# Performance work log

Measured on AMD Instinct MI355X. Metric: run time of the kernel, lower is better.

## Reference

```python
import jax, jax.numpy as jnp
import numpy as np

K_NEIGHBORS = 32  # nsample

def setup_inputs() -> dict:
    key = jax.random.key(0)
    ks = jax.random.split(key, 16)
    B, C, N = 4, 3, 4096
    def w(k, shape):
        return jax.random.normal(k, shape, dtype=jnp.float32) * 0.05
    inp = {"x": jax.random.normal(ks[0], (B, C, N), dtype=jnp.float32)}
    # three scale MLPs share shapes -> stack along leading scale axis (s=3)
    inp["sW0"] = w(ks[1], (3, 64, 3));    inp["sb0"] = w(ks[2], (3, 64))
    inp["sW1"] = w(ks[3], (3, 64, 64));   inp["sb1"] = w(ks[4], (3, 64))
    inp["sW2"] = w(ks[5], (3, 128, 64));  inp["sb2"] = w(ks[6], (3, 128))
    inp["gW0"] = w(ks[7], (256, 384));    inp["gb0"] = w(ks[8], (256,))
    inp["gW1"] = w(ks[9], (1024, 256));   inp["gb1"] = w(ks[10], (1024,))
    inp["mW0"] = w(ks[11], (256, 1024));  inp["mb0"] = w(ks[12], (256,))
    inp["mW1"] = w(ks[13], (128, 256));   inp["mb1"] = w(ks[14], (128,))
    return inp

def _knn_idx(x, k):
    # x: [B, 3, N] channels-first points; k nearest neighbors excluding self
    pts = jnp.swapaxes(x, 1, 2)                       # [B, N, 3]
    sq = jnp.sum(pts * pts, axis=-1)                  # [B, N]
    d = sq[:, :, None] + sq[:, None, :] - 2.0 * jnp.einsum('bnc,bmc->bnm', pts, pts)
    _, idx = jax.lax.top_k(-d, k + 1)                 # nearest first (self at 0)
    return idx[:, :, 1:]                              # [B, N, k]

def reference(x, sW0, sb0, sW1, sb1, sW2, sb2, gW0, gb0, gW1, gb1, mW0, mb0, mW1, mb1):
    B, C, N = x.shape
    # radius is unused by sample_and_group_knn -> all three scales share knn idx
    idx = _knn_idx(x, K_NEIGHBORS)                    # [B, N, K]
    # gather: per-batch x[:, idx[b]] -> [B, C, N, K]
    g = jax.vmap(lambda xf, i: xf[:, i])(x, idx)
    # three shared-weight 1x1-conv MLPs, batched over scale axis s
    h = jax.nn.relu(jnp.einsum('bcnk,soc->sbonk', g, sW0) + sb0[:, None, :, None, None])
    h = jax.nn.relu(jnp.einsum('sbcnk,soc->sbonk', h, sW1) + sb1[:, None, :, None, None])
    h = jax.nn.relu(jnp.einsum('sbcnk,soc->sbonk', h, sW2) + sb2[:, None, :, None, None])
    p = jnp.max(h, axis=-1)                           # [3, B, 128, N] max over neighbors
    point = jnp.moveaxis(p, 0, 1).reshape(B, 3 * p.shape[2], N)  # concat scales -> [B, 384, N]
    gf = jax.nn.relu(jnp.einsum('bcn,oc->bon', point, gW0) + gb0[None, :, None])
    gf = jax.nn.relu(jnp.einsum('bcn,oc->bon', gf, gW1) + gb1[None, :, None])     # [B,1024,N]
    msf = jax.nn.relu(jnp.einsum('bcn,oc->bon', gf, mW0) + mb0[None, :, None])
    msf = jax.nn.relu(jnp.einsum('bcn,oc->bon', msf, mW1) + mb1[None, :, None])   # [B,128,N]
    global_feature = jnp.max(gf, axis=-1)             # [B, 1024]
    return (global_feature, msf)
```

## Files before the change

### kernel.cpp

```cpp
#include <hip/hip_runtime.h>
#include <hip/hip_bf16.h>

#define NPTS 4096
#define KNN  32

typedef __attribute__((ext_vector_type(8))) short short8;
typedef __attribute__((ext_vector_type(4))) float floatx4;
typedef unsigned short u16x2 __attribute__((ext_vector_type(2)));

__device__ __forceinline__ unsigned short f2bf(float f) {
    unsigned u = __float_as_uint(f);
    u = (u + 0x7FFFu + ((u >> 16) & 1u)) >> 16;
    return (unsigned short)u;
}

__global__ __launch_bounds__(256) void prep_all(
    const float* __restrict__ x, float4* __restrict__ pts4,
    const float* __restrict__ gW0, const float* __restrict__ gW1,
    const float* __restrict__ mW0, const float* __restrict__ mW1,
    unsigned short* __restrict__ Wb0, unsigned short* __restrict__ Wb1,
    unsigned short* __restrict__ Wb2, unsigned short* __restrict__ Wb3)
{
    const int blk = blockIdx.x, t = threadIdx.x;
    if (blk < 64) {
        const int i = blk * 256 + t;
        const int b = i >> 12, n = i & (NPTS - 1);
        const float* xb = x + (size_t)b * 3 * NPTS;
        const float qx = xb[n], qy = xb[NPTS + n], qz = xb[2 * NPTS + n];
        pts4[i] = make_float4(qx, qy, qz, qx * qx + qy * qy + qz * qz);
    } else {
        const int wi = (blk - 64) * 256 + t;
        float v; unsigned short* dst;
        if (wi < 98304)       { v = gW0[wi];          dst = Wb0 + wi; }
        else if (wi < 360448) { v = gW1[wi - 98304];  dst = Wb1 + (wi - 98304); }
        else if (wi < 622592) { v = mW0[wi - 360448]; dst = Wb2 + (wi - 360448); }
        else                  { v = mW1[wi - 622592]; dst = Wb3 + (wi - 622592); }
        *dst = f2bf(v);
    }
}

__global__ __launch_bounds__(256) void knn_kernel12(const float4* __restrict__ pts4,
                                                    int* __restrict__ knn_out)
{
    __shared__ unsigned sred[2][4];
    __shared__ unsigned long long C[256];
    __shared__ unsigned ccnt;

    const int t = threadIdx.x, wid = t >> 6, lane = t & 63;
    const int q = blockIdx.x, b = q >> 12, n = q & (NPTS - 1);
    const float4* P = pts4 + ((size_t)b << 12);
    const float4 s = P[n];
    const float px = s.x, py = s.y, pz = s.z, sqn = s.w;

    if (t == 0) ccnt = 0u;

    unsigned key[16];
    #pragma unroll
    for (int g = 0; g < 4; ++g) {
        float4 c0 = P[((g * 4 + 0) << 8) + t];
        float4 c1 = P[((g * 4 + 1) << 8) + t];
        float4 c2 = P[((g * 4 + 2) << 8) + t];
        float4 c3 = P[((g * 4 + 3) << 8) + t];
        float d0 = (sqn + c0.w) - 2.0f * (px * c0.x + py * c0.y + pz * c0.z);
        float d1 = (sqn + c1.w) - 2.0f * (px * c1.x + py * c1.y + pz * c1.z);
        float d2 = (sqn + c2.w) - 2.0f * (px * c2.x + py * c2.y + pz * c2.z);
        float d3 = (sqn + c3.w) - 2.0f * (px * c3.x + py * c3.y + pz * c3.z);
        unsigned u0 = __float_as_uint(d0), u1 = __float_as_uint(d1);
        unsigned u2 = __float_as_uint(d2), u3 = __float_as_uint(d3);
        key[g * 4 + 0] = (u0 & 0x80000000u) ? ~u0 : (u0 | 0x80000000u);
        key[g * 4 + 1] = (u1 & 0x80000000u) ? ~u1 : (u1 | 0x80000000u);
        key[g * 4 + 2] = (u2 & 0x80000000u) ? ~u2 : (u2 | 0x80000000u);
        key[g * 4 + 3] = (u3 & 0x80000000u) ? ~u3 : (u3 | 0x80000000u);
    }

    int pp = 0;
    auto countLE = [&](unsigned thr) -> unsigned {
        unsigned c = 0;
        #pragma unroll
        for (int r = 0; r < 16; ++r)
            c += (unsigned)__popcll(__ballot(key[r] <= thr));
        if (lane == 0) sred[pp & 1][wid] = c;
        __syncthreads();
        const unsigned g = sred[pp & 1][0] + sred[pp & 1][1] +
                           sred[pp & 1][2] + sred[pp & 1][3];
        ++pp;
        return g;
    };

    unsigned lo = 0x100u, hi = 0x1FEu;
    for (int it = 0; it < 8; ++it) {
        const unsigned mid = (lo + hi) >> 1;
        const unsigned g = countLE((mid << 23) | 0x7FFFFFu);
        if (g >= 33u) hi = mid; else lo = mid + 1u;
    }
    unsigned loK = lo << 23;
    unsigned hiK = (lo << 23) | 0x7FFFFFu;
    unsigned cntF = countLE(hiK);
    while (cntF > 256u && loK < hiK) {
        const unsigned midK = loK + ((hiK - loK) >> 1);
        const unsigned c = countLE(midK);
        if (c >= 33u) { hiK = midK; cntF = c; } else loK = midK + 1u;
    }
    const unsigned thrF = hiK;

    #pragma unroll
    for (int r = 0; r < 16; ++r) {
        if (key[r] <= thrF) {
            unsigned p = atomicAdd(&ccnt, 1u);
            if (p < 256u)
                C[p] = ((unsigned long long)key[r] << 32) |
                       (unsigned)((r << 8) + t);
        }
    }
    __syncthreads();

    int nc = (int)ccnt; if (nc > 256) nc = 256;
    if (t < nc) {
        const unsigned long long me = C[t];
        int rank = 0;
        for (int j = 0; j < nc; ++j) rank += (C[j] < me) ? 1 : 0;
        if (rank >= 1 && rank <= KNN)
            knn_out[(size_t)q * KNN + (rank - 1)] = (int)(me & 0xFFFFFFFFu);
    }
}

__global__ __launch_bounds__(256) void pointmlp_kernel(
    const float* __restrict__ x,
    const float* __restrict__ sW0, const float* __restrict__ sb0,
    const float* __restrict__ sW1, const float* __restrict__ sb1,
    const float* __restrict__ sW2, const float* __restrict__ sb2,
    unsigned short* __restrict__ F)
{
    __shared__ __align__(16) float BUF[8192];
    __shared__ __align__(16) float h1s[64 * 36];
    __shared__ float b1s[64];
    __shared__ float b2s[128];
    __shared__ float pts[3 * 33];

    const int t = threadIdx.x;
    const int s = blockIdx.y;
    const int tile = blockIdx.x;
    const int b = tile >> 7;
    const int j0 = (tile & 127) << 5;
    const float* xb = x + (size_t)b * 3 * NPTS;

    if (t < 192) BUF[t] = sW0[s * 192 + t];
    else if (t < 256) BUF[t] = sb0[s * 64 + (t - 192)];
    if (t < 64) b1s[t] = sb1[s * 64 + t];
    if (t < 128) b2s[t] = sb2[s * 128 + t];
    if (t < 96) { int c = t >> 5, p = t & 31; pts[c * 33 + p] = xb[c * NPTS + j0 + p]; }
    {
        const float* W1 = sW1 + (size_t)s * 4096;
        int o = t & 63, q = t >> 6;
        #pragma unroll
        for (int r = 0; r < 4; ++r) {
            float4 w = *(const float4*)(W1 + o * 64 + q * 16 + r * 4);
            int i = q * 16 + r * 4;
            BUF[256 + (i + 0) * 64 + o] = w.x;
            BUF[256 + (i + 1) * 64 + o] = w.y;
            BUF[256 + (i + 2) * 64 + o] = w.z;
            BUF[256 + (i + 3) * 64 + o] = w.w;
        }
    }
    __syncthreads();
    const int o = t & 63, pg = t >> 6;
    float* h0 = BUF + 4352;
    {
        float w0 = BUF[o * 3], w1 = BUF[o * 3 + 1], w2 = BUF[o * 3 + 2], bb = BUF[192 + o];
        #pragma unroll
        for (int p = 0; p < 8; ++p) {
            int pp = pg * 8 + p;
            float a = bb + w0 * pts[pp] + w1 * pts[33 + pp] + w2 * pts[66 + pp];
            h0[o * 36 + pp] = fmaxf(a, 0.0f);
        }
    }
    __syncthreads();
    {
        float acc[8];
        #pragma unroll
        for (int p = 0; p < 8; ++p) acc[p] = b1s[o];
        for (int i = 0; i < 64; ++i) {
            float w = BUF[256 + i * 64 + o];
            float4 ha = *(const float4*)&h0[i * 36 + pg * 8];
            float4 hb = *(const float4*)&h0[i * 36 + pg * 8 + 4];
            acc[0] += w * ha.x; acc[1] += w * ha.y; acc[2] += w * ha.z; acc[3] += w * ha.w;
            acc[4] += w * hb.x; acc[5] += w * hb.y; acc[6] += w * hb.z; acc[7] += w * hb.w;
        }
        #pragma unroll
        for (int p = 0; p < 8; ++p) h1s[o * 36 + pg * 8 + p] = fmaxf(acc[p], 0.0f);
    }
    __syncthreads();
    {
        const float* W2 = sW2 + (size_t)s * 8192;
        int o2 = t & 127, q = t >> 7;
        #pragma unroll
        for (int r = 0; r < 8; ++r) {
            float4 w = *(const float4*)(W2 + o2 * 64 + q * 32 + r * 4);
            int i = q * 32 + r * 4;
            BUF[(i + 0) * 128 + o2] = w.x;
            BUF[(i + 1) * 128 + o2] = w.y;
            BUF[(i + 2) * 128 + o2] = w.z;
            BUF[(i + 3) * 128 + o2] = w.w;
        }
    }
    __syncthreads();
    {
        int o2 = t & 127, ph = t >> 7;
        float acc[16];
        #pragma unroll
        for (int p = 0; p < 16; ++p) acc[p] = b2s[o2];
        for (int i = 0; i < 64; ++i) {
            float w = BUF[i * 128 + o2];
            float4 ha = *(const float4*)&h1s[i * 36 + ph * 16];
            float4 hb = *(const float4*)&h1s[i * 36 + ph * 16 + 4];
            float4 hc = *(const float4*)&h1s[i * 36 + ph * 16 + 8];
            float4 hd = *(const float4*)&h1s[i * 36 + ph * 16 + 12];
            acc[0]  += w * ha.x; acc[1]  += w * ha.y; acc[2]  += w * ha.z; acc[3]  += w * ha.w;
            acc[4]  += w * hb.x; acc[5]  += w * hb.y; acc[6]  += w * hb.z; acc[7]  += w * hb.w;
            acc[8]  += w * hc.x; acc[9]  += w * hc.y; acc[10] += w * hc.z; acc[11] += w * hc.w;
            acc[12] += w * hd.x; acc[13] += w * hd.y; acc[14] += w * hd.z; acc[15] += w * hd.w;
        }
        #pragma unroll
        for (int p = 0; p < 16; ++p) {
            int j = j0 + ph * 16 + p;
            F[((size_t)b * NPTS + j) * 384 + s * 128 + o2] = f2bf(fmaxf(acc[p], 0.0f));
        }
    }
}

__global__ __launch_bounds__(192) void maxgather_bf16(
    const unsigned short* __restrict__ F, const int* __restrict__ knn,
    unsigned short* __restrict__ pt)
{
    __shared__ int idxS[KNN];
    const int q = blockIdx.x;
    const int b = q >> 12;
    const int t = threadIdx.x;
    if (t < KNN) idxS[t] = knn[(size_t)q * KNN + t];
    __syncthreads();
    const unsigned short* Fb = F + (size_t)b * NPTS * 384 + t * 2;
    u16x2 m = (u16x2)0;
    #pragma unroll 8
    for (int k = 0; k < KNN; ++k) {
        u16x2 v = *(const u16x2*)(Fb + (size_t)idxS[k] * 384);
        m = __builtin_elementwise_max(m, v);
    }
    *(u16x2*)(pt + (size_t)q * 384 + t * 2) = m;
}

template<int DO_ROWMAX>
__global__ __launch_bounds__(256) void gemm_bf16(
    const unsigned short* __restrict__ Wb, const unsigned short* __restrict__ Bt,
    const float* __restrict__ bias, void* __restrict__ outp,
    float* __restrict__ gfeat, int M, int K)
{
    __shared__ __align__(16) unsigned short As[128 * 40];
    __shared__ __align__(16) unsigned short Bs[128 * 40];
    __shared__ float biasS[128];
    __shared__ int redI[128];

    const int t = threadIdx.x;
    const int b = blockIdx.z;
    const int m0 = blockIdx.x * 128;
    const int n0 = blockIdx.y * 128;
    if (t < 128) biasS[t] = bias[m0 + t];
    if (DO_ROWMAX && t < 128) redI[t] = 0;

    const int wave = t >> 6, lane = t & 63, quad = lane >> 4, l15 = lane & 15;
    const int wr = wave >> 1, wc = wave & 1;

    const int am = t & 127, akh = t >> 7;
    const unsigned short* Wp = Wb + (size_t)(m0 + am) * K + akh * 16;
    const int bn = t >> 2, bq = t & 3;
    const unsigned short* Bp = Bt + ((size_t)b * NPTS + n0) * K;

    floatx4 acc[16];
    #pragma unroll
    for (int i = 0; i < 16; ++i) acc[i] = (floatx4){0.f, 0.f, 0.f, 0.f};

    const int nk = K >> 5;
    for (int kt = 0; kt < nk; ++kt) {
        const int k0 = kt << 5;
        uint4 av0 = *(const uint4*)(Wp + k0);
        uint4 av1 = *(const uint4*)(Wp + k0 + 8);
        uint4 bv0 = *(const uint4*)(Bp + (size_t)bn * K + k0 + bq * 8);
        uint4 bv1 = *(const uint4*)(Bp + (size_t)(bn + 64) * K + k0 + bq * 8);
        __syncthreads();
        {
            uint4* dst = (uint4*)&As[am * 40 + akh * 16];
            dst[0] = av0;
            dst[1] = av1;
            *(uint4*)&Bs[bn * 40 + bq * 8] = bv0;
            *(uint4*)&Bs[(bn + 64) * 40 + bq * 8] = bv1;
        }
        __syncthreads();
        short8 af[4], bfv[4];
        #pragma unroll
        for (int i = 0; i < 4; ++i)
            af[i] = *(const short8*)&As[(wr * 64 + i * 16 + l15) * 40 + quad * 8];
        #pragma unroll
        for (int j = 0; j < 4; ++j)
            bfv[j] = *(const short8*)&Bs[(wc * 64 + j * 16 + l15) * 40 + quad * 8];
        #pragma unroll
        for (int i = 0; i < 4; ++i)
            #pragma unroll
            for (int j = 0; j < 4; ++j)
                acc[i * 4 + j] = __builtin_amdgcn_mfma_f32_16x16x32_bf16(
                    af[i], bfv[j], acc[i * 4 + j], 0, 0, 0);
    }

    #pragma unroll
    for (int i = 0; i < 4; ++i) {
        const int mbase = wr * 64 + i * 16 + quad * 4;
        float rm0 = 0.f, rm1 = 0.f, rm2 = 0.f, rm3 = 0.f;
        #pragma unroll
        for (int j = 0; j < 4; ++j) {
            const int n = n0 + wc * 64 + j * 16 + l15;
            float v0 = fmaxf(acc[i * 4 + j][0] + biasS[mbase + 0], 0.f);
            float v1 = fmaxf(acc[i * 4 + j][1] + biasS[mbase + 1], 0.f);
            float v2 = fmaxf(acc[i * 4 + j][2] + biasS[mbase + 2], 0.f);
            float v3 = fmaxf(acc[i * 4 + j][3] + biasS[mbase + 3], 0.f);
            if (DO_ROWMAX) {
                rm0 = fmaxf(rm0, v0); rm1 = fmaxf(rm1, v1);
                rm2 = fmaxf(rm2, v2); rm3 = fmaxf(rm3, v3);
            }
            ushort4 pk;
            pk.x = f2bf(v0); pk.y = f2bf(v1); pk.z = f2bf(v2); pk.w = f2bf(v3);
            *(ushort4*)((unsigned short*)outp +
                        ((size_t)b * NPTS + n) * M + m0 + mbase) = pk;
        }
        if (DO_ROWMAX) {
            atomicMax(&redI[mbase + 0], __float_as_int(rm0));
            atomicMax(&redI[mbase + 1], __float_as_int(rm1));
            atomicMax(&redI[mbase + 2], __float_as_int(rm2));
            atomicMax(&redI[mbase + 3], __float_as_int(rm3));
        }
    }
    if (DO_ROWMAX) {
        __syncthreads();
        if (t < 128)
            atomicMax((int*)&gfeat[(size_t)b * 1024 + m0 + t], redI[t]);
    }
}

__global__ __launch_bounds__(256) void fused_head(
    const unsigned short* __restrict__ Wb2, const unsigned short* __restrict__ Wb3,
    const float* __restrict__ mb0, const float* __restrict__ mb1,
    const unsigned short* __restrict__ gft, float* __restrict__ outp)
{
    __shared__ __align__(16) unsigned short As[256 * 40];
    __shared__ __align__(16) unsigned short Bs[64 * 40];
    __shared__ __align__(16) unsigned short H[64 * 264];
    __shared__ float b0s[256];
    __shared__ float b1s[128];

    const int t = threadIdx.x;
    const int n0 = blockIdx.x * 64;
    const int b = blockIdx.y;
    b0s[t] = mb0[t];
    if (t < 128) b1s[t] = mb1[t];

    const int wave = t >> 6, lane = t & 63, quad = lane >> 4, l15 = lane & 15;

    const unsigned short* Ap = Wb2 + (size_t)t * 1024;
    const int bn = t >> 2, bq = t & 3;
    const unsigned short* Bp = gft + ((size_t)b * NPTS + n0) * 1024;

    floatx4 acc[16];
    #pragma unroll
    for (int i = 0; i < 16; ++i) acc[i] = (floatx4){0.f, 0.f, 0.f, 0.f};

    for (int kt = 0; kt < 32; ++kt) {
        const int k0 = kt << 5;
        uint4 a0 = *(const uint4*)(Ap + k0);
        uint4 a1 = *(const uint4*)(Ap + k0 + 8);
        uint4 a2 = *(const uint4*)(Ap + k0 + 16);
        uint4 a3 = *(const uint4*)(Ap + k0 + 24);
        uint4 bv = *(const uint4*)(Bp + (size_t)bn * 1024 + k0 + bq * 8);
        __syncthreads();
        *(uint4*)&As[t * 40 + 0]  = a0;
        *(uint4*)&As[t * 40 + 8]  = a1;
        *(uint4*)&As[t * 40 + 16] = a2;
        *(uint4*)&As[t * 40 + 24] = a3;
        *(uint4*)&Bs[bn * 40 + bq * 8] = bv;
        __syncthreads();
        short8 af[4], bfv[4];
        #pragma unroll
        for (int i = 0; i < 4; ++i)
            af[i] = *(const short8*)&As[(wave * 64 + i * 16 + l15) * 40 + quad * 8];
        #pragma unroll
        for (int j = 0; j < 4; ++j)
            bfv[j] = *(const short8*)&Bs[(j * 16 + l15) * 40 + quad * 8];
        #pragma unroll
        for (int i = 0; i < 4; ++i)
            #pragma unroll
            for (int j = 0; j < 4; ++j)
                acc[i * 4 + j] = __builtin_amdgcn_mfma_f32_16x16x32_bf16(
                    af[i], bfv[j], acc[i * 4 + j], 0, 0, 0);
    }
    #pragma unroll
    for (int i = 0; i < 4; ++i) {
        const int mbase = wave * 64 + i * 16 + quad * 4;
        #pragma unroll
        for (int j = 0; j < 4; ++j) {
            const int nl = j * 16 + l15;
            ushort4 pk;
            pk.x = f2bf(fmaxf(acc[i * 4 + j][0] + b0s[mbase + 0], 0.f));
            pk.y = f2bf(fmaxf(acc[i * 4 + j][1] + b0s[mbase + 1], 0.f));
            pk.z = f2bf(fmaxf(acc[i * 4 + j][2] + b0s[mbase + 2], 0.f));
            pk.w = f2bf(fmaxf(acc[i * 4 + j][3] + b0s[mbase + 3], 0.f));
            *(ushort4*)&H[nl * 264 + mbase] = pk;
        }
    }

    floatx4 acc2[8];
    #pragma unroll
    for (int i = 0; i < 8; ++i) acc2[i] = (floatx4){0.f, 0.f, 0.f, 0.f};
    const int am2 = t & 127, ah = t >> 7;

    for (int kt = 0; kt < 8; ++kt) {
        const int k0 = kt << 5;
        uint4 a0 = *(const uint4*)(Wb3 + (size_t)am2 * 256 + k0 + ah * 16);
        uint4 a1 = *(const uint4*)(Wb3 + (size_t)am2 * 256 + k0 + ah * 16 + 8);
        __syncthreads();
        *(uint4*)&As[am2 * 40 + ah * 16]     = a0;
        *(uint4*)&As[am2 * 40 + ah * 16 + 8] = a1;
        __syncthreads();
        short8 af2[2], bf2[4];
        #pragma unroll
        for (int i = 0; i < 2; ++i)
            af2[i] = *(const short8*)&As[(wave * 32 + i * 16 + l15) * 40 + quad * 8];
        #pragma unroll
        for (int j = 0; j < 4; ++j)
            bf2[j] = *(const short8*)&H[(j * 16 + l15) * 264 + k0 + quad * 8];
        #pragma unroll
        for (int i = 0; i < 2; ++i)
            #pragma unroll
            for (int j = 0; j < 4; ++j)
                acc2[i * 4 + j] = __builtin_amdgcn_mfma_f32_16x16x32_bf16(
                    af2[i], bf2[j], acc2[i * 4 + j], 0, 0, 0);
    }
    #pragma unroll
    for (int i = 0; i < 2; ++i) {
        const int m2 = wave * 32 + i * 16 + quad * 4;
        #pragma unroll
        for (int j = 0; j < 4; ++j) {
            const int n = n0 + j * 16 + l15;
            float* o = outp + ((size_t)b * 128 + m2) * NPTS + n;
            o[0 * NPTS] = fmaxf(acc2[i * 4 + j][0] + b1s[m2 + 0], 0.f);
            o[1 * NPTS] = fmaxf(acc2[i * 4 + j][1] + b1s[m2 + 1], 0.f);
            o[2 * NPTS] = fmaxf(acc2[i * 4 + j][2] + b1s[m2 + 2], 0.f);
            o[3 * NPTS] = fmaxf(acc2[i * 4 + j][3] + b1s[m2 + 3], 0.f);
        }
    }
}

extern "C" void kernel_launch(void* const* d_in, const int* in_sizes, int n_in,
                              void* d_out, int out_size, void* d_ws, size_t ws_size,
                              hipStream_t stream)
{
    const float* x   = (const float*)d_in[0];
    const float* sW0 = (const float*)d_in[1];
    const float* sb0 = (const float*)d_in[2];
    const float* sW1 = (const float*)d_in[3];
    const float* sb1 = (const float*)d_in[4];
    const float* sW2 = (const float*)d_in[5];
    const float* sb2 = (const float*)d_in[6];
    const float* gW0 = (const float*)d_in[7];
    const float* gb0 = (const float*)d_in[8];
    const float* gW1 = (const float*)d_in[9];
    const float* gb1 = (const float*)d_in[10];
    const float* mW0 = (const float*)d_in[11];
    const float* mb0 = (const float*)d_in[12];
    const float* mW1 = (const float*)d_in[13];
    const float* mb1 = (const float*)d_in[14];
    float* outp = (float*)d_out;

    char* ws = (char*)d_ws;
    int*            idx     = (int*)(ws);
    float4*         pts4    = (float4*)(ws + 2097152u);
    unsigned short* Wb0     = (unsigned short*)(ws + 2359296u);
    unsigned short* Wb1     = (unsigned short*)(ws + 2555904u);
    unsigned short* Wb2     = (unsigned short*)(ws + 3080192u);
    unsigned short* Wb3     = (unsigned short*)(ws + 3604480u);
    unsigned short* F       = (unsigned short*)(ws + 4194304u);
    unsigned short* point_t = (unsigned short*)(ws + 18874368u);
    unsigned short* gf0t    = (unsigned short*)(ws + 33554432u);
    unsigned short* gft     = (unsigned short*)(ws + 50331648u);

    prep_all<<<dim3(2624), dim3(256), 0, stream>>>(
        x, pts4, gW0, gW1, mW0, mW1, Wb0, Wb1, Wb2, Wb3);
    knn_kernel12<<<dim3(16384), dim3(256), 0, stream>>>(pts4, idx);
    pointmlp_kernel<<<dim3(512, 3), dim3(256), 0, stream>>>(
        x, sW0, sb0, sW1, sb1, sW2, sb2, F);
    maxgather_bf16<<<dim3(16384), dim3(192), 0, stream>>>(F, idx, point_t);
    gemm_bf16<0><<<dim3(2, 32, 4), dim3(256), 0, stream>>>(
        Wb0, point_t, gb0, gf0t, nullptr, 256, 384);
    gemm_bf16<1><<<dim3(8, 32, 4), dim3(256), 0, stream>>>(
        Wb1, gf0t, gb1, gft, outp, 1024, 256);
    fused_head<<<dim3(64, 4), dim3(256), 0, stream>>>(
        Wb2, Wb3, mb0, mb1, gft, outp + 4096);
}
```

Before: 286.8 us.

## Port per-point MLP to bf16 MFMA and reuse KNN bisection count

The per-point scale MLP layers 1 and 2 now run on bf16 MFMA 16x16x32 instructions. The weights are converted to bf16 once in the prep kernel and staged in padded LDS tiles, replacing the scalar fp32 FMA loops. Separately, the KNN radix bisection reuses the count it recorded at the upper bound instead of issuing one more counting pass. The MLP change cuts compute and LDS traffic, at the cost of bf16 rounding of intermediate activations.

```diff
diff --git a/kernel.cpp b/kernel.cpp
--- a/kernel.cpp
+++ b/kernel.cpp
@@ -18,8 +18,10 @@
     const float* __restrict__ x, float4* __restrict__ pts4,
     const float* __restrict__ gW0, const float* __restrict__ gW1,
     const float* __restrict__ mW0, const float* __restrict__ mW1,
+    const float* __restrict__ sW1, const float* __restrict__ sW2,
     unsigned short* __restrict__ Wb0, unsigned short* __restrict__ Wb1,
-    unsigned short* __restrict__ Wb2, unsigned short* __restrict__ Wb3)
+    unsigned short* __restrict__ Wb2, unsigned short* __restrict__ Wb3,
+    unsigned short* __restrict__ Wb4, unsigned short* __restrict__ Wb5)
 {
     const int blk = blockIdx.x, t = threadIdx.x;
     if (blk < 64) {
@@ -34,12 +36,14 @@
         if (wi < 98304)       { v = gW0[wi];          dst = Wb0 + wi; }
         else if (wi < 360448) { v = gW1[wi - 98304];  dst = Wb1 + (wi - 98304); }
         else if (wi < 622592) { v = mW0[wi - 360448]; dst = Wb2 + (wi - 360448); }
-        else                  { v = mW1[wi - 622592]; dst = Wb3 + (wi - 622592); }
+        else if (wi < 655360) { v = mW1[wi - 622592]; dst = Wb3 + (wi - 622592); }
+        else if (wi < 667648) { v = sW1[wi - 655360]; dst = Wb4 + (wi - 655360); }
+        else                  { v = sW2[wi - 667648]; dst = Wb5 + (wi - 667648); }
         *dst = f2bf(v);
     }
 }
 
-__global__ __launch_bounds__(256) void knn_kernel12(const float4* __restrict__ pts4,
+__global__ __launch_bounds__(256) void knn_kernel13(const float4* __restrict__ pts4,
                                                     int* __restrict__ knn_out)
 {
     __shared__ unsigned sred[2][4];
@@ -87,15 +91,15 @@
         return g;
     };
 
-    unsigned lo = 0x100u, hi = 0x1FEu;
+    unsigned lo = 0x100u, hi = 0x1FEu, cntHi = 4096u;
     for (int it = 0; it < 8; ++it) {
         const unsigned mid = (lo + hi) >> 1;
         const unsigned g = countLE((mid << 23) | 0x7FFFFFu);
-        if (g >= 33u) hi = mid; else lo = mid + 1u;
+        if (g >= 33u) { hi = mid; cntHi = g; } else lo = mid + 1u;
     }
     unsigned loK = lo << 23;
     unsigned hiK = (lo << 23) | 0x7FFFFFu;
-    unsigned cntF = countLE(hiK);
+    unsigned cntF = cntHi;
     while (cntF > 256u && loK < hiK) {
         const unsigned midK = loK + ((hiK - loK) >> 1);
         const unsigned c = countLE(midK);
@@ -124,17 +128,19 @@
     }
 }
 
-__global__ __launch_bounds__(256) void pointmlp_kernel(
+__global__ __launch_bounds__(256) void pointmlp_mfma(
     const float* __restrict__ x,
     const float* __restrict__ sW0, const float* __restrict__ sb0,
-    const float* __restrict__ sW1, const float* __restrict__ sb1,
-    const float* __restrict__ sW2, const float* __restrict__ sb2,
+    const unsigned short* __restrict__ W1b, const float* __restrict__ sb1,
+    const unsigned short* __restrict__ W2b, const float* __restrict__ sb2,
     unsigned short* __restrict__ F)
 {
-    __shared__ __align__(16) float BUF[8192];
-    __shared__ __align__(16) float h1s[64 * 36];
-    __shared__ float b1s[64];
-    __shared__ float b2s[128];
+    __shared__ __align__(16) unsigned short W1s[64 * 72];
+    __shared__ __align__(16) unsigned short W2s[128 * 72];
+    __shared__ __align__(16) unsigned short h0T[32 * 72];
+    __shared__ __align__(16) unsigned short h1T[32 * 72];
+    __shared__ float W0s[192];
+    __shared__ float b0s[64], b1s[64], b2s[128];
     __shared__ float pts[3 * 33];
 
     const int t = threadIdx.x;
@@ -144,86 +150,88 @@
     const int j0 = (tile & 127) << 5;
     const float* xb = x + (size_t)b * 3 * NPTS;
 
-    if (t < 192) BUF[t] = sW0[s * 192 + t];
-    else if (t < 256) BUF[t] = sb0[s * 64 + (t - 192)];
-    if (t < 64) b1s[t] = sb1[s * 64 + t];
+    if (t < 192) W0s[t] = sW0[s * 192 + t];
+    if (t < 64) b0s[t] = sb0[s * 64 + t];
+    if (t >= 64 && t < 128) b1s[t - 64] = sb1[s * 64 + (t - 64)];
     if (t < 128) b2s[t] = sb2[s * 128 + t];
     if (t < 96) { int c = t >> 5, p = t & 31; pts[c * 33 + p] = xb[c * NPTS + j0 + p]; }
     {
-        const float* W1 = sW1 + (size_t)s * 4096;
-        int o = t & 63, q = t >> 6;
-        #pragma unroll
-        for (int r = 0; r < 4; ++r) {
-            float4 w = *(const float4*)(W1 + o * 64 + q * 16 + r * 4);
-            int i = q * 16 + r * 4;
-            BUF[256 + (i + 0) * 64 + o] = w.x;
-            BUF[256 + (i + 1) * 64 + o] = w.y;
-            BUF[256 + (i + 2) * 64 + o] = w.z;
-            BUF[256 + (i + 3) * 64 + o] = w.w;
-        }
+        const int o = t & 63, qq = t >> 6;
+        const unsigned short* src = W1b + (size_t)s * 4096 + o * 64 + qq * 16;
+        *(uint4*)&W1s[o * 72 + qq * 16]     = *(const uint4*)src;
+        *(uint4*)&W1s[o * 72 + qq * 16 + 8] = *(const uint4*)(src + 8);
+    }
+    {
+        const int o2 = t & 127, hh = t >> 7;
+        const unsigned short* src = W2b + (size_t)s * 8192 + o2 * 64 + hh * 32;
+        *(uint4*)&W2s[o2 * 72 + hh * 32]      = *(const uint4*)src;
+        *(uint4*)&W2s[o2 * 72 + hh * 32 + 8]  = *(const uint4*)(src + 8);
+        *(uint4*)&W2s[o2 * 72 + hh * 32 + 16] = *(const uint4*)(src + 16);
+        *(uint4*)&W2s[o2 * 72 + hh * 32 + 24] = *(const uint4*)(src + 24);
     }
     __syncthreads();
-    const int o = t & 63, pg = t >> 6;
-    float* h0 = BUF + 4352;
+
     {
-        float w0 = BUF[o * 3], w1 = BUF[o * 3 + 1], w2 = BUF[o * 3 + 2], bb = BUF[192 + o];
-        #pragma unroll
-        for (int p = 0; p < 8; ++p) {
-            int pp = pg * 8 + p;
-            float a = bb + w0 * pts[pp] + w1 * pts[33 + pp] + w2 * pts[66 + pp];
-            h0[o * 36 + pp] = fmaxf(a, 0.0f);
-        }
+        const int p = t & 31, og = t >> 5;
+        const float xx = pts[p], yy = pts[33 + p], zz = pts[66 + p];
+        unsigned short hv[8];
+        #pragma unroll
+        for (int r = 0; r < 8; ++r) {
+            const int o = og * 8 + r;
+            float a = b0s[o] + W0s[o * 3] * xx + W0s[o * 3 + 1] * yy
+                    + W0s[o * 3 + 2] * zz;
+            hv[r] = f2bf(fmaxf(a, 0.0f));
+        }
+        *(uint4*)&h0T[p * 72 + og * 8] = *(const uint4*)hv;
     }
     __syncthreads();
+
+    const int w = t >> 6, lane = t & 63, quad = lane >> 4, l15 = lane & 15;
+
     {
-        float acc[8];
-        #pragma unroll
-        for (int p = 0; p < 8; ++p) acc[p] = b1s[o];
-        for (int i = 0; i < 64; ++i) {
-            float w = BUF[256 + i * 64 + o];
-            float4 ha = *(const float4*)&h0[i * 36 + pg * 8];
-            float4 hb = *(const float4*)&h0[i * 36 + pg * 8 + 4];
-            acc[0] += w * ha.x; acc[1] += w * ha.y; acc[2] += w * ha.z; acc[3] += w * ha.w;
-            acc[4] += w * hb.x; acc[5] += w * hb.y; acc[6] += w * hb.z; acc[7] += w * hb.w;
-        }
-        #pragma unroll
-        for (int p = 0; p < 8; ++p) h1s[o * 36 + pg * 8 + p] = fmaxf(acc[p], 0.0f);
+        #pragma unroll
+        for (int ni = 0; ni < 2; ++ni) {
+            floatx4 acc = (floatx4){0.f, 0.f, 0.f, 0.f};
+            #pragma unroll
+            for (int k0 = 0; k0 < 2; ++k0) {
+                short8 aF = *(const short8*)&W1s[(w * 16 + l15) * 72 + k0 * 32 + quad * 8];
+                short8 bF = *(const short8*)&h0T[(ni * 16 + l15) * 72 + k0 * 32 + quad * 8];
+                acc = __builtin_amdgcn_mfma_f32_16x16x32_bf16(aF, bF, acc, 0, 0, 0);
+            }
+            const int m0 = w * 16 + quad * 4;
+            const int p = ni * 16 + l15;
+            ushort4 pk;
+            pk.x = f2bf(fmaxf(acc[0] + b1s[m0 + 0], 0.f));
+            pk.y = f2bf(fmaxf(acc[1] + b1s[m0 + 1], 0.f));
+            pk.z = f2bf(fmaxf(acc[2] + b1s[m0 + 2], 0.f));
+            pk.w = f2bf(fmaxf(acc[3] + b1s[m0 + 3], 0.f));
+            *(ushort4*)&h1T[p * 72 + m0] = pk;
+        }
     }
     __syncthreads();
+
     {
-        const float* W2 = sW2 + (size_t)s * 8192;
-        int o2 = t & 127, q = t >> 7;
-        #pragma unroll
-        for (int r = 0; r < 8; ++r) {
-            float4 w = *(const float4*)(W2 + o2 * 64 + q * 32 + r * 4);
-            int i = q * 32 + r * 4;
-            BUF[(i + 0) * 128 + o2] = w.x;
-            BUF[(i + 1) * 128 + o2] = w.y;
-            BUF[(i + 2) * 128 + o2] = w.z;
-            BUF[(i + 3) * 128 + o2] = w.w;
-        }
-    }
-    __syncthreads();
-    {
-        int o2 = t & 127, ph = t >> 7;
-        float acc[16];
-        #pragma unroll
-        for (int p = 0; p < 16; ++p) acc[p] = b2s[o2];
-        for (int i = 0; i < 64; ++i) {
-            float w = BUF[i * 128 + o2];
-            float4 ha = *(const float4*)&h1s[i * 36 + ph * 16];
-            float4 hb = *(const float4*)&h1s[i * 36 + ph * 16 + 4];
-            float4 hc = *(const float4*)&h1s[i * 36 + ph * 16 + 8];
-            float4 hd = *(const float4*)&h1s[i * 36 + ph * 16 + 12];
-            acc[0]  += w * ha.x; acc[1]  += w * ha.y; acc[2]  += w * ha.z; acc[3]  += w * ha.w;
-            acc[4]  += w * hb.x; acc[5]  += w * hb.y; acc[6]  += w * hb.z; acc[7]  += w * hb.w;
-            acc[8]  += w * hc.x; acc[9]  += w * hc.y; acc[10] += w * hc.z; acc[11] += w * hc.w;
-            acc[12] += w * hd.x; acc[13] += w * hd.y; acc[14] += w * hd.z; acc[15] += w * hd.w;
-        }
-        #pragma unroll
-        for (int p = 0; p < 16; ++p) {
-            int j = j0 + ph * 16 + p;
-            F[((size_t)b * NPTS + j) * 384 + s * 128 + o2] = f2bf(fmaxf(acc[p], 0.0f));
+        #pragma unroll
+        for (int mi = 0; mi < 2; ++mi) {
+            const int m0 = (w * 2 + mi) * 16;
+            #pragma unroll
+            for (int ni = 0; ni < 2; ++ni) {
+                floatx4 acc = (floatx4){0.f, 0.f, 0.f, 0.f};
+                #pragma unroll
+                for (int k0 = 0; k0 < 2; ++k0) {
+                    short8 aF = *(const short8*)&W2s[(m0 + l15) * 72 + k0 * 32 + quad * 8];
+                    short8 bF = *(const short8*)&h1T[(ni * 16 + l15) * 72 + k0 * 32 + quad * 8];
+                    acc = __builtin_amdgcn_mfma_f32_16x16x32_bf16(aF, bF, acc, 0, 0, 0);
+                }
+                const int o2 = m0 + quad * 4;
+                const int j = j0 + ni * 16 + l15;
+                ushort4 pk;
+                pk.x = f2bf(fmaxf(acc[0] + b2s[o2 + 0], 0.f));
+                pk.y = f2bf(fmaxf(acc[1] + b2s[o2 + 1], 0.f));
+                pk.z = f2bf(fmaxf(acc[2] + b2s[o2 + 2], 0.f));
+                pk.w = f2bf(fmaxf(acc[3] + b2s[o2 + 3], 0.f));
+                *(ushort4*)&F[((size_t)b * NPTS + j) * 384 + s * 128 + o2] = pk;
+            }
         }
     }
 }
@@ -483,16 +491,18 @@
     unsigned short* Wb1     = (unsigned short*)(ws + 2555904u);
     unsigned short* Wb2     = (unsigned short*)(ws + 3080192u);
     unsigned short* Wb3     = (unsigned short*)(ws + 3604480u);
+    unsigned short* Wb4     = (unsigned short*)(ws + 3670016u);
+    unsigned short* Wb5     = (unsigned short*)(ws + 3694592u);
     unsigned short* F       = (unsigned short*)(ws + 4194304u);
     unsigned short* point_t = (unsigned short*)(ws + 18874368u);
     unsigned short* gf0t    = (unsigned short*)(ws + 33554432u);
     unsigned short* gft     = (unsigned short*)(ws + 50331648u);
 
-    prep_all<<<dim3(2624), dim3(256), 0, stream>>>(
-        x, pts4, gW0, gW1, mW0, mW1, Wb0, Wb1, Wb2, Wb3);
-    knn_kernel12<<<dim3(16384), dim3(256), 0, stream>>>(pts4, idx);
-    pointmlp_kernel<<<dim3(512, 3), dim3(256), 0, stream>>>(
-        x, sW0, sb0, sW1, sb1, sW2, sb2, F);
+    prep_all<<<dim3(2768), dim3(256), 0, stream>>>(
+        x, pts4, gW0, gW1, mW0, mW1, sW1, sW2, Wb0, Wb1, Wb2, Wb3, Wb4, Wb5);
+    knn_kernel13<<<dim3(16384), dim3(256), 0, stream>>>(pts4, idx);
+    pointmlp_mfma<<<dim3(512, 3), dim3(256), 0, stream>>>(
+        x, sW0, sb0, Wb4, sb1, Wb5, sb2, F);
     maxgather_bf16<<<dim3(16384), dim3(192), 0, stream>>>(F, idx, point_t);
     gemm_bf16<0><<<dim3(2, 32, 4), dim3(256), 0, stream>>>(
         Wb0, point_t, gb0, gf0t, nullptr, 256, 384);
```

Measured after the change: 269.8 us. 5.9% less time.
